# Optimization experiments

Measured on AMD Instinct MI355X. Metric: run time of the kernel, lower is better.

## Reference

```python
import jax, jax.numpy as jnp
import numpy as np

DEPTH = 6; HEADS = 6; DIM = 384; HD = DIM // HEADS
WS = 14; WINDOW_BLOCKS = (0, 1, 3, 4)
IMG = 512; PATCH = 16; GRID = IMG // PATCH        # 32x32 token grid
PRE_GRID = 14                                      # 224 // 16 pretrain grid
SCALE = HD ** -0.5


def layer_norm(x, w, b, eps=1e-5):
    u = x.mean(-1, keepdims=True)
    s = ((x - u) ** 2).mean(-1, keepdims=True)
    return (x - u) / jnp.sqrt(s + eps) * w + b


def get_rel_pos(size, rel_pos):
    # q_size == k_size here; relative coords in [0, 2*size-2]
    coords = jnp.arange(size)[:, None] - jnp.arange(size)[None, :] + (size - 1)
    return rel_pos[coords]  # (size, size, HD)


def attention(x, qkv_w, qkv_b, proj_w, proj_b, rel_h, rel_w):
    B, H, W, C = x.shape
    N = H * W
    qkv = (x.reshape(B, N, C) @ qkv_w.T + qkv_b).reshape(B, N, 3, HEADS, HD)
    qkv = jnp.moveaxis(qkv, 2, 0).transpose(0, 1, 3, 2, 4)  # (3,B,h,N,d)
    q, k, v = qkv[0], qkv[1], qkv[2]
    attn = jnp.einsum('bhqd,bhkd->bhqk', q * SCALE, k)
    # decomposed relative position bias (ViTDet add_decomposed_rel_pos)
    Rh = get_rel_pos(H, rel_h)  # (H,H,d)
    Rw = get_rel_pos(W, rel_w)  # (W,W,d)
    rq = q.reshape(B, HEADS, H, W, HD)
    bias_h = jnp.einsum('bnhwc,hkc->bnhwk', rq, Rh)  # (B,h,H,W,H)
    bias_w = jnp.einsum('bnhwc,wkc->bnhwk', rq, Rw)  # (B,h,H,W,W)
    attn = (attn.reshape(B, HEADS, H, W, H, W)
            + bias_h[..., :, None] + bias_w[..., None, :]).reshape(B, HEADS, N, N)
    attn = jax.nn.softmax(attn, axis=-1)
    out = jnp.einsum('bhqk,bhkd->bhqd', attn, v)
    out = out.transpose(0, 2, 1, 3).reshape(B, H, W, C)
    return out @ proj_w.T + proj_b


def window_partition(x, ws):
    B, H, W, C = x.shape
    pad_h = (ws - H % ws) % ws
    pad_w = (ws - W % ws) % ws
    x = jnp.pad(x, ((0, 0), (0, pad_h), (0, pad_w), (0, 0)))
    Hp, Wp = H + pad_h, W + pad_w
    x = x.reshape(B, Hp // ws, ws, Wp // ws, ws, C)
    x = x.transpose(0, 1, 3, 2, 4, 5).reshape(-1, ws, ws, C)
    return x, Hp, Wp


def window_unpartition(win, ws, Hp, Wp, H, W):
    B = win.shape[0] // ((Hp // ws) * (Wp // ws))
    x = win.reshape(B, Hp // ws, Wp // ws, ws, ws, -1)
    x = x.transpose(0, 1, 3, 2, 4, 5).reshape(B, Hp, Wp, -1)
    return x[:, :H, :W]


def block(x, p, windowed):
    shortcut = x
    x = layer_norm(x, p['n1w'], p['n1b'])
    if windowed:
        H, W = x.shape[1], x.shape[2]
        x, Hp, Wp = window_partition(x, WS)
    x = attention(x, p['qw'], p['qb'], p['pw'], p['pb'], p['rh'], p['rw'])
    if windowed:
        x = window_unpartition(x, WS, Hp, Wp, H, W)
    x = shortcut + x
    h = layer_norm(x, p['n2w'], p['n2b'])
    h = jax.nn.gelu(h @ p['f1w'].T + p['f1b'], approximate=False)
    return x + h @ p['f2w'].T + p['f2b']


def vit_forward(x, patch_w, patch_b, pos_embed, norm1_w, norm1_b, qkv_w, qkv_b,
                proj_w, proj_b, norm2_w, norm2_b, fc1_w, fc1_b, fc2_w, fc2_b,
                rel_pos_h, rel_pos_w):
    y = jax.lax.conv_general_dilated(
        x, patch_w, (PATCH, PATCH), 'VALID',
        dimension_numbers=('NCHW', 'OIHW', 'NCHW'))
    y = y.transpose(0, 2, 3, 1) + patch_b  # (B, GRID, GRID, DIM)
    # abs pos embed: bicubic resize from pretrain 14x14 grid to 32x32
    pos = pos_embed.reshape(1, PRE_GRID, PRE_GRID, DIM)
    pos = jax.image.resize(pos, (1, GRID, GRID, DIM), 'bicubic')
    y = y + pos
    for i in range(DEPTH):
        windowed = i in WINDOW_BLOCKS
        L = 2 * WS - 1 if windowed else 2 * GRID - 1
        p = dict(n1w=norm1_w[i], n1b=norm1_b[i], qw=qkv_w[i], qb=qkv_b[i],
                 pw=proj_w[i], pb=proj_b[i], rh=rel_pos_h[i, :L], rw=rel_pos_w[i, :L],
                 n2w=norm2_w[i], n2b=norm2_b[i], f1w=fc1_w[i], f1b=fc1_b[i],
                 f2w=fc2_w[i], f2b=fc2_b[i])
        y = block(y, p, windowed)
    return y.transpose(0, 3, 1, 2)  # (B, DIM, GRID, GRID) 'last_feat'


def setup_inputs() -> dict:
    key = jax.random.key(0)
    ks = jax.random.split(key, 10)
    B = 4
    std = 0.02
    f32 = jnp.float32
    return {
        'x': jax.random.normal(ks[0], (B, 3, IMG, IMG), f32),
        'patch_w': jax.random.normal(ks[1], (DIM, 3, PATCH, PATCH), f32) * 0.05,
        'patch_b': jnp.zeros((DIM,), f32),
        'pos_embed': jax.random.normal(ks[2], (1, PRE_GRID * PRE_GRID, DIM), f32) * std,
        'norm1_w': jnp.ones((DEPTH, DIM), f32),
        'norm1_b': jnp.zeros((DEPTH, DIM), f32),
        'qkv_w': jax.random.normal(ks[3], (DEPTH, 3 * DIM, DIM), f32) * std,
        'qkv_b': jnp.zeros((DEPTH, 3 * DIM), f32),
        'proj_w': jax.random.normal(ks[4], (DEPTH, DIM, DIM), f32) * std,
        'proj_b': jnp.zeros((DEPTH, DIM), f32),
        'norm2_w': jnp.ones((DEPTH, DIM), f32),
        'norm2_b': jnp.zeros((DEPTH, DIM), f32),
        'fc1_w': jax.random.normal(ks[5], (DEPTH, 4 * DIM, DIM), f32) * std,
        'fc1_b': jnp.zeros((DEPTH, 4 * DIM), f32),
        'fc2_w': jax.random.normal(ks[6], (DEPTH, DIM, 4 * DIM), f32) * std,
        'fc2_b': jnp.zeros((DEPTH, DIM), f32),
        'rel_pos_h': jax.random.normal(ks[7], (DEPTH, 2 * GRID - 1, HD), f32) * std,
        'rel_pos_w': jax.random.normal(ks[8], (DEPTH, 2 * GRID - 1, HD), f32) * std,
    }


def reference(x, patch_w, patch_b, pos_embed, norm1_w, norm1_b, qkv_w, qkv_b,
              proj_w, proj_b, norm2_w, norm2_b, fc1_w, fc1_b, fc2_w, fc2_b,
              rel_pos_h, rel_pos_w):
    return vit_forward(x, patch_w, patch_b, pos_embed, norm1_w, norm1_b, qkv_w, qkv_b,
                       proj_w, proj_b, norm2_w, norm2_b, fc1_w, fc1_b, fc2_w, fc2_b,
                       rel_pos_h, rel_pos_w)
```

## Files before the change

### kernel.cpp

```cpp
#include <hip/hip_runtime.h>
#include <math.h>

#define B_SZ 4
#define DIM 384
#define HEADS 6
#define HD 64
#define NTOK 4096
#define WS 14
#define NWIN 36
#define WTOK 196

typedef unsigned short u16;
typedef __bf16 bf16_t;
typedef bf16_t bf16x8 __attribute__((ext_vector_type(8)));
typedef float f32x4 __attribute__((ext_vector_type(4)));

__device__ __forceinline__ float bf2f(unsigned u) { return __uint_as_float(u << 16); }
__device__ __forceinline__ u16 f2bf(float f) {
    unsigned u = __float_as_uint(f);
    unsigned r = (u + 0x7fffu + ((u >> 16) & 1u)) >> 16;
    return (u16)r;
}

__device__ __forceinline__ void ldsload16(const u16* g, u16* l) {
    __builtin_amdgcn_global_load_lds(
        (const __attribute__((address_space(1))) unsigned int*)g,
        (__attribute__((address_space(3))) unsigned int*)l, 16, 0, 0);
}

__device__ __forceinline__ int swz(int r) { return (r ^ (r >> 2)) & 3; }

__global__ __launch_bounds__(256) void w2b_all_kernel(
        const float* __restrict__ p0, const float* __restrict__ p1,
        const float* __restrict__ p2, const float* __restrict__ p3,
        const float* __restrict__ p4, const float* __restrict__ p5,
        u16* __restrict__ d) {
    int i = blockIdx.x * 256 + threadIdx.x;
    const float* s; int off;
    if      (i <   294912) { s = p0; off = 0; }
    else if (i <  2949120) { s = p1; off = 294912; }
    else if (i <  3833856) { s = p2; off = 2949120; }
    else if (i <  7372800) { s = p3; off = 3833856; }
    else if (i < 10911744) { s = p4; off = 7372800; }
    else if (i < 10918656) { s = p5; off = 10911744; }
    else return;
    d[i] = f2bf(s[i - off]);
}

__global__ __launch_bounds__(256) void im2col_kernel(const float* __restrict__ x,
                                                     u16* __restrict__ col) {
    size_t idx = (size_t)blockIdx.x * 256 + threadIdx.x;
    if (idx >= (size_t)NTOK * 768) return;
    int kk = (int)(idx % 768);
    int p  = (int)(idx / 768);
    int b  = p / 1024;
    int ph = (p % 1024) / 32;
    int pw = p % 32;
    int c = kk / 256;
    int r = kk % 256;
    int i = r / 16, j = r % 16;
    col[idx] = f2bf(x[(size_t)b * 3 * 512 * 512 + (size_t)c * 512 * 512 +
                      (size_t)(ph * 16 + i) * 512 + (pw * 16 + j)]);
}

__device__ inline float cubic_keys(float x) {
    x = fabsf(x);
    if (x <= 1.f) return ((1.5f * x - 2.5f) * x) * x + 1.f;
    if (x < 2.f)  return ((-0.5f * x + 2.5f) * x - 4.f) * x + 2.f;
    return 0.f;
}

__global__ __launch_bounds__(256) void pos_resize_kernel(const float* __restrict__ pe,
                                                         float* __restrict__ posr) {
    int idx = blockIdx.x * 256 + threadIdx.x;
    if (idx >= 1024 * 384) return;
    int c = idx % 384;
    int g = idx / 384;
    int gy = g / 32, gx = g % 32;
    float wy[14], wx[14];
    float sy = (gy + 0.5f) * (14.f / 32.f) - 0.5f;
    float sx = (gx + 0.5f) * (14.f / 32.f) - 0.5f;
    float toty = 0.f, totx = 0.f;
    #pragma unroll
    for (int k = 0; k < 14; ++k) {
        wy[k] = cubic_keys(sy - (float)k); toty += wy[k];
        wx[k] = cubic_keys(sx - (float)k); totx += wx[k];
    }
    float val = 0.f;
    #pragma unroll 1
    for (int iy = 0; iy < 14; ++iy) {
        if (wy[iy] == 0.f) continue;
        float row = 0.f;
        for (int ix = 0; ix < 14; ++ix) {
            if (wx[ix] == 0.f) continue;
            row += wx[ix] * pe[(iy * 14 + ix) * 384 + c];
        }
        val += wy[iy] * row;
    }
    posr[idx] = val / (toty * totx);
}

__global__ __launch_bounds__(64) void epi_ln_kernel(const float* __restrict__ P,
        const float* __restrict__ bias, const float* __restrict__ posr,
        float* __restrict__ y, int addy, int nsk,
        const float* __restrict__ lw, const float* __restrict__ lb,
        u16* __restrict__ lnout, float* __restrict__ outT)
{
    int tok = blockIdx.x, t = threadIdx.x;
    size_t base = (size_t)tok * 384;
    float v[6];
    float s = 0.f;
    #pragma unroll
    for (int i = 0; i < 6; ++i) {
        int c = t + 64 * i;
        float val = bias[c];
        #pragma unroll 1
        for (int sk = 0; sk < nsk; ++sk)
            val += P[(size_t)sk * 1572864 + base + c];
        if (posr) val += posr[(size_t)(tok & 1023) * 384 + c];
        if (addy) val += y[base + c];
        v[i] = val; s += val;
    }
    if (outT) {
        int b = tok >> 10, g = tok & 1023;
        #pragma unroll
        for (int i = 0; i < 6; ++i) {
            int c = t + 64 * i;
            outT[((size_t)(b * 384 + c)) * 1024 + g] = v[i];
        }
        return;
    }
    #pragma unroll
    for (int i = 0; i < 6; ++i) y[base + t + 64 * i] = v[i];
    if (!lnout) return;
    #pragma unroll
    for (int off = 32; off > 0; off >>= 1) s += __shfl_xor(s, off);
    float mean = s * (1.f / 384.f);
    float vs = 0.f;
    #pragma unroll
    for (int i = 0; i < 6; ++i) { float d = v[i] - mean; vs += d * d; }
    #pragma unroll
    for (int off = 32; off > 0; off >>= 1) vs += __shfl_xor(vs, off);
    float inv = rsqrtf(vs * (1.f / 384.f) + 1e-5f);
    u16* orow = lnout + base;
    #pragma unroll
    for (int i = 0; i < 6; ++i) {
        int c = t + 64 * i;
        orow[c] = f2bf((v[i] - mean) * inv * lw[c] + lb[c]);
    }
}

__global__ __launch_bounds__(256) void mfma_gemm3(
        const u16* __restrict__ A, const u16* __restrict__ Wt,
        const float* __restrict__ bias,
        float* __restrict__ outf, u16* __restrict__ outb,
        float* __restrict__ outp,
        int M, int N, int K, int act, int ksplit)
{
    __shared__ u16 As[8192];
    __shared__ u16 Bs[4096];
    int t = threadIdx.x;
    int lane = t & 63, wave = t >> 6;
    int wm = (wave >> 1) * 64, wn = (wave & 1) * 32;
    int m0 = blockIdx.y * 128, n0 = blockIdx.x * 64;
    int ks = blockIdx.z * ksplit, ke = ks + ksplit;

    int r0 = t >> 2,        c0 = ((t & 3) ^ swz(t >> 2)) * 8;
    int r1 = 64 + (t >> 2), c1 = ((t & 3) ^ swz(64 + (t >> 2))) * 8;
    const u16* a0 = A + (size_t)(m0 + r0) * K + c0;
    const u16* a1 = A + (size_t)(m0 + r1) * K + c1;
    const u16* b0 = Wt + (size_t)(n0 + r0) * K + c0;
    u16* asd0 = &As[wave * 512];
    u16* asd1 = &As[2048 + wave * 512];
    u16* bsd0 = &Bs[wave * 512];

    f32x4 acc[4][2] = {};
    int row_a = wm + (lane & 15);
    int row_b = wn + (lane & 15);
    int lq = lane >> 4;

    for (int k0 = ks; k0 < ke; k0 += 64) {
        ldsload16(a0 + k0, asd0);
        ldsload16(a1 + k0, asd1);
        ldsload16(b0 + k0, bsd0);
        ldsload16(a0 + k0 + 32, asd0 + 4096);
        ldsload16(a1 + k0 + 32, asd1 + 4096);
        ldsload16(b0 + k0 + 32, bsd0 + 2048);
        __syncthreads();
        #pragma unroll
        for (int hf = 0; hf < 2; ++hf) {
            bf16x8 af[4], bfr[2];
            #pragma unroll
            for (int i = 0; i < 4; ++i) {
                int r = row_a + i * 16;
                af[i] = *(const bf16x8*)&As[hf * 4096 + r * 32 + ((lq ^ swz(r)) * 8)];
            }
            #pragma unroll
            for (int j = 0; j < 2; ++j) {
                int r = row_b + j * 16;
                bfr[j] = *(const bf16x8*)&Bs[hf * 2048 + r * 32 + ((lq ^ swz(r)) * 8)];
            }
            #pragma unroll
            for (int i = 0; i < 4; ++i)
                #pragma unroll
                for (int j = 0; j < 2; ++j)
                    acc[i][j] = __builtin_amdgcn_mfma_f32_16x16x32_bf16(
                        af[i], bfr[j], acc[i][j], 0, 0, 0);
        }
        __syncthreads();
    }

    int colq = lane & 15, rowq = (lane >> 4) * 4;
    if (outp) {
        float* pp = outp + (size_t)blockIdx.z * M * N;
        #pragma unroll
        for (int i = 0; i < 4; ++i) {
            #pragma unroll
            for (int rr = 0; rr < 4; ++rr) {
                int m = m0 + wm + i * 16 + rowq + rr;
                size_t mo = (size_t)m * N;
                #pragma unroll
                for (int j = 0; j < 2; ++j) {
                    int n = n0 + wn + j * 16 + colq;
                    pp[mo + n] = acc[i][j][rr];
                }
            }
        }
        return;
    }
    #pragma unroll
    for (int i = 0; i < 4; ++i) {
        #pragma unroll
        for (int rr = 0; rr < 4; ++rr) {
            int m = m0 + wm + i * 16 + rowq + rr;
            size_t mo = (size_t)m * N;
            #pragma unroll
            for (int j = 0; j < 2; ++j) {
                int n = n0 + wn + j * 16 + colq;
                float v = acc[i][j][rr] + bias[n];
                if (act)  v = 0.5f * v * (1.f + erff(v * 0.70710678118654752f));
                if (outf) outf[mo + n] = v;
                if (outb) outb[mo + n] = f2bf(v);
            }
        }
    }
}

template<int N, int W>
__global__ __launch_bounds__(256) void attn_mfma(const u16* __restrict__ qkv,
        const u16* __restrict__ qkb, const float* __restrict__ rh,
        const float* __restrict__ rw, u16* __restrict__ outb)
{
    constexpr int JS = (W == 32) ? 64 : 32;
    constexpr int L  = (W == 32) ? 63 : 27;
    constexpr int CTR = W - 1;
    __shared__ u16 KV[7168];
    __shared__ u16 bhl[64 * 66];
    __shared__ u16 bwl[64 * 66];
    __shared__ u16 Qt[64 * 66];

    u16* Ks = KV;
    u16* Vt = KV + 2048;
    u16* Pb = KV + 4608;
    u16* Rt = KV;

    int t = threadIdx.x, lane = t & 63, wave = t >> 6;
    int quad = lane >> 4, l15 = lane & 15;
    int uh = blockIdx.x, qb0 = blockIdx.y * 64;
    int h = uh % HEADS, u = uh / HEADS;
    size_t tbase = (size_t)u * 1024;
    int wb_ = u / 9, wr = u - wb_ * 9;
    int wy = wr / 3, wx = wr - wy * 3;

    auto rowptr = [&](int lq) -> const u16* {
        if constexpr (W == 32) {
            return qkv + (tbase + lq) * 1152;
        } else {
            int iy = lq / WS, ix = lq - iy * WS;
            int gy = wy * WS + iy, gx = wx * WS + ix;
            if (gy < 32 || gx < 32) {
                if (gy < 32 && gx < 32)
                    return qkv + (size_t)(wb_ * 1024 + gy * 32 + gx) * 1152;
            }
            return qkb;
        }
    };

    {
        int q = t & 63, ch0 = (t >> 6) * 16;
        int qc = qb0 + q; if (qc >= N) qc = N - 1;
        const u16* qp = rowptr(qc) + h * 64 + ch0;
        uint4 a = *(const uint4*)qp;
        uint4 b = *(const uint4*)(qp + 8);
        u16 vals[16];
        *(uint4*)vals = a; *(uint4*)(vals + 8) = b;
        #pragma unroll
        for (int c = 0; c < 16; ++c)
            Qt[(ch0 + c) * 66 + q] = ((qb0 + q) < N) ? vals[c] : (u16)0;
    }

    #pragma unroll
    for (int table = 0; table < 2; ++table) {
        __syncthreads();
        const float* tab = table ? rw : rh;
        for (int idx = t; idx < JS * 8; idx += 256) {
            int j = idx >> 3, cc0 = (idx & 7) * 8;
            u16 tmp[8];
            if (j < L) {
                const float* src = tab + (size_t)j * 64 + cc0;
                #pragma unroll
                for (int c = 0; c < 8; ++c) tmp[c] = f2bf(src[c]);
            } else {
                #pragma unroll
                for (int c = 0; c < 8; ++c) tmp[c] = 0;
            }
            *(uint4*)&Rt[j * 72 + cc0] = *(uint4*)tmp;
        }
        __syncthreads();
        if (wave < JS / 16) {
            int jt = wave;
            bf16x8 af0 = *(const bf16x8*)&Rt[(jt * 16 + l15) * 72 + quad * 8];
            bf16x8 af1 = *(const bf16x8*)&Rt[(jt * 16 + l15) * 72 + 32 + quad * 8];
            u16* dst = table ? bwl : bhl;
            #pragma unroll
            for (int qt = 0; qt < 4; ++qt) {
                bf16x8 qf0, qf1;
                u16* p0 = (u16*)&qf0; u16* p1 = (u16*)&qf1;
                #pragma unroll
                for (int z = 0; z < 8; ++z) {
                    p0[z] = Qt[(quad * 8 + z) * 66 + qt * 16 + l15];
                    p1[z] = Qt[(32 + quad * 8 + z) * 66 + qt * 16 + l15];
                }
                f32x4 acc = {};
                acc = __builtin_amdgcn_mfma_f32_16x16x32_bf16(af0, qf0, acc, 0, 0, 0);
                acc = __builtin_amdgcn_mfma_f32_16x16x32_bf16(af1, qf1, acc, 0, 0, 0);
                #pragma unroll
                for (int r = 0; r < 4; ++r)
                    dst[(qt * 16 + l15) * 66 + jt * 16 + quad * 4 + r] = f2bf(acc[r]);
            }
        }
    }
    __syncthreads();

    bf16x8 qf[2];
    #pragma unroll
    for (int hc = 0; hc < 2; ++hc) {
        u16* qv = (u16*)&qf[hc];
        #pragma unroll
        for (int j = 0; j < 8; ++j)
            qv[j] = Qt[(hc * 32 + quad * 8 + j) * 66 + wave * 16 + l15];
    }
    int qme = wave * 16 + l15;
    int qq = qb0 + qme; if (qq >= N) qq = N - 1;
    int qh = qq / W, qw = qq - qh * W;
    float bwreg[2][4];
    if constexpr (W == 32) {
        #pragma unroll
        for (int kc2 = 0; kc2 < 2; ++kc2)
            #pragma unroll
            for (int r = 0; r < 4; ++r) {
                int keyl = kc2 * 16 + quad * 4 + r;
                bwreg[kc2][r] = bf2f(bwl[qme * 66 + (qw - keyl + CTR)]);
            }
    }

    f32x4 of[4] = {};
    float lsum = 0.f;
    constexpr int NKT = (N + 31) / 32;

    for (int kt = 0; kt < NKT; ++kt) {
        int kb = kt * 32;
        __syncthreads();
        {
            int p = wave * 64 + lane;
            int key = p >> 3;
            int c8 = (p & 7) ^ (key & 7);
            int kc = kb + key; if (kc >= N) kc = N - 1;
            ldsload16(rowptr(kc) + 384 + h * 64 + c8 * 8, &Ks[wave * 512]);
        }
        {
            int k = t & 31, ch0 = (t >> 5) * 8;
            int kc = kb + k; if (kc >= N) kc = N - 1;
            const u16* vp = rowptr(kc) + 768 + h * 64 + ch0;
            uint4 vv = *(const uint4*)vp;
            u16 tmp[8]; *(uint4*)tmp = vv;
            #pragma unroll
            for (int c = 0; c < 8; ++c) Vt[(ch0 + c) * 40 + k] = tmp[c];
        }
        __syncthreads();

        f32x4 st[2] = {};
        #pragma unroll
        for (int hc = 0; hc < 2; ++hc) {
            #pragma unroll
            for (int kc2 = 0; kc2 < 2; ++kc2) {
                int key = kc2 * 16 + l15;
                int c8 = hc * 4 + quad;
                int p = key * 8 + (c8 ^ (key & 7));
                bf16x8 kf = *(const bf16x8*)&Ks[p * 8];
                st[kc2] = __builtin_amdgcn_mfma_f32_16x16x32_bf16(
                    kf, qf[hc], st[kc2], 0, 0, 0);
            }
        }
        float bh_t = 0.f;
        if constexpr (W == 32) bh_t = bf2f(bhl[qme * 66 + (qh - (kb >> 5) + CTR)]);
        #pragma unroll
        for (int kc2 = 0; kc2 < 2; ++kc2) {
            #pragma unroll
            for (int r = 0; r < 4; ++r) {
                int keyl = kc2 * 16 + quad * 4 + r;
                int key = kb + keyl;
                float b;
                if constexpr (W == 32) {
                    b = bh_t + bwreg[kc2][r];
                } else {
                    int kk2 = (key < N) ? key : (N - 1);
                    int kh = kk2 / W, kw = kk2 - kh * W;
                    b = bf2f(bhl[qme * 66 + (qh - kh + CTR)]) +
                        bf2f(bwl[qme * 66 + (qw - kw + CTR)]);
                }
                float p = __expf(fmaf(st[kc2][r], 0.125f, b));
                if (key >= N) p = 0.f;
                lsum += p;
                Pb[wave * 640 + l15 * 40 + keyl] = f2bf(p);
            }
        }
        bf16x8 pf = *(const bf16x8*)&Pb[wave * 640 + l15 * 40 + quad * 8];
        #pragma unroll
        for (int ca = 0; ca < 4; ++ca) {
            bf16x8 vf = *(const bf16x8*)&Vt[(ca * 16 + l15) * 40 + quad * 8];
            of[ca] = __builtin_amdgcn_mfma_f32_16x16x32_bf16(
                vf, pf, of[ca], 0, 0, 0);
        }
    }

    lsum += __shfl_xor(lsum, 16);
    lsum += __shfl_xor(lsum, 32);
    float inv = 1.f / lsum;
    int q = qb0 + qme;
    if (q < N) {
        u16* op;
        if constexpr (W == 32) {
            op = outb + (tbase + q) * 384 + h * 64;
        } else {
            int iy = q / WS, ix = q - iy * WS;
            int gy = wy * WS + iy, gx = wx * WS + ix;
            if (gy >= 32 || gx >= 32) return;
            op = outb + (size_t)(wb_ * 1024 + gy * 32 + gx) * 384 + h * 64;
        }
        #pragma unroll
        for (int ca = 0; ca < 4; ++ca)
            #pragma unroll
            for (int r = 0; r < 4; ++r)
                op[ca * 16 + quad * 4 + r] = f2bf(of[ca][r] * inv);
    }
}

static inline void launch_gemm(const u16* A, const u16* W, const float* bias,
                               float* outf, u16* outb,
                               int M, int N, int K, int act, hipStream_t s) {
    dim3 g(N / 64, M / 128, 1);
    mfma_gemm3<<<g, 256, 0, s>>>(A, W, bias, outf, outb, nullptr, M, N, K, act, K);
}

static inline void launch_gemm_sk(const u16* A, const u16* W, float* P,
                                  int M, int N, int K, int SK, hipStream_t s) {
    dim3 g(N / 64, M / 128, SK);
    mfma_gemm3<<<g, 256, 0, s>>>(A, W, nullptr, nullptr, nullptr, P,
                                 M, N, K, 0, K / SK);
}

extern "C" void kernel_launch(void* const* d_in, const int* in_sizes, int n_in,
                              void* d_out, int out_size, void* d_ws, size_t ws_size,
                              hipStream_t stream) {
    const float* x      = (const float*)d_in[0];
    const float* patchw = (const float*)d_in[1];
    const float* patchb = (const float*)d_in[2];
    const float* pos    = (const float*)d_in[3];
    const float* n1w    = (const float*)d_in[4];
    const float* n1b    = (const float*)d_in[5];
    const float* qkvw   = (const float*)d_in[6];
    const float* qkvb   = (const float*)d_in[7];
    const float* pw     = (const float*)d_in[8];
    const float* pb     = (const float*)d_in[9];
    const float* n2w    = (const float*)d_in[10];
    const float* n2b    = (const float*)d_in[11];
    const float* f1w    = (const float*)d_in[12];
    const float* f1b    = (const float*)d_in[13];
    const float* f2w    = (const float*)d_in[14];
    const float* f2b    = (const float*)d_in[15];
    const float* rph    = (const float*)d_in[16];
    const float* rpw    = (const float*)d_in[17];
    float* out = (float*)d_out;

    float* y   = (float*)d_ws;
    u16* attb  = (u16*)(y + 1572864);
    u16* mlpb  = attb + 1572864;
    u16* lnb   = mlpb + 6291456;
    u16* qkvx  = lnb + 1572864;
    u16* rsrv  = qkvx + 4718592;
    u16* wb    = rsrv + 7864320;
    float* posr = (float*)(wb + 10918656);

    u16* colb  = rsrv;
    float* P_patch = (float*)attb;
    float* P_pf    = (float*)qkvx;

    u16* wb_patch = wb;
    u16* wb_qkv   = wb + 294912;
    u16* wb_pw    = wb + 2949120;
    u16* wb_f1    = wb + 3833856;
    u16* wb_f2    = wb + 7372800;
    u16* wqb      = wb + 10911744;

    w2b_all_kernel<<<(10918656 + 255) / 256, 256, 0, stream>>>(
        patchw, qkvw, pw, f1w, f2w, qkvb, wb);
    pos_resize_kernel<<<1536, 256, 0, stream>>>(pos, posr);

    {
        size_t tot = (size_t)NTOK * 768;
        im2col_kernel<<<(int)((tot + 255) / 256), 256, 0, stream>>>(x, colb);
        launch_gemm_sk(colb, wb_patch, P_patch, NTOK, 384, 768, 2, stream);
        epi_ln_kernel<<<NTOK, 64, 0, stream>>>(P_patch, patchb, posr, y, 0, 2,
                                               n1w, n1b, lnb, nullptr);
    }

    for (int i = 0; i < 6; ++i) {
        bool windowed = (i == 0 || i == 1 || i == 3 || i == 4);
        const float* rh = rph + (size_t)i * 63 * 64;
        const float* rw = rpw + (size_t)i * 63 * 64;
        launch_gemm(lnb, wb_qkv + (size_t)i * 442368, qkvb + i * 1152,
                    nullptr, qkvx, NTOK, 1152, 384, 0, stream);
        if (windowed) {
            attn_mfma<WTOK, WS><<<dim3(NWIN * HEADS, 4), 256, 0, stream>>>(
                qkvx, wqb + i * 1152, rh, rw, attb);
        } else {
            attn_mfma<1024, 32><<<dim3(B_SZ * HEADS, 16), 256, 0, stream>>>(
                qkvx, wqb + i * 1152, rh, rw, attb);
        }
        launch_gemm_sk(attb, wb_pw + (size_t)i * 147456, P_pf,
                       NTOK, 384, 384, 2, stream);
        epi_ln_kernel<<<NTOK, 64, 0, stream>>>(P_pf, pb + i * 384, nullptr, y, 1, 2,
                                               n2w + i * 384, n2b + i * 384, lnb,
                                               nullptr);
        launch_gemm(lnb, wb_f1 + (size_t)i * 589824, f1b + i * 1536,
                    nullptr, mlpb, NTOK, 1536, 384, 1, stream);
        launch_gemm_sk(mlpb, wb_f2 + (size_t)i * 589824, P_pf,
                       NTOK, 384, 1536, 4, stream);
        if (i < 5)
            epi_ln_kernel<<<NTOK, 64, 0, stream>>>(P_pf, f2b + i * 384, nullptr, y,
                                                   1, 4, n1w + (i + 1) * 384,
                                                   n1b + (i + 1) * 384, lnb, nullptr);
        else
            epi_ln_kernel<<<NTOK, 64, 0, stream>>>(P_pf, f2b + i * 384, nullptr, y,
                                                   1, 4, nullptr, nullptr, nullptr,
                                                   out);
    }
}
```

Before: 797.8 us.

## Double-buffer K/V tiles in attention, merge setup kernels, reduce fc2 split-K

The attention kernel now double-buffers its K and V tiles in shared memory. The next tile's K is issued via global_load_lds and V is prefetched into registers while the current tile is computed, leaving one barrier per iteration instead of two. The weight-conversion, positional-resize and im2col kernels are merged into a single launch to cut launch overhead. The fc2 split-K factor drops from 4 to 2, which halves partial-sum traffic but gives the GEMM fewer blocks, and the larger LDS footprint may lower attention occupancy.

After: 775.6 us. 2.8% less time.

```diff
diff --git a/kernel.cpp b/kernel.cpp
--- a/kernel.cpp
+++ b/kernel.cpp
@@ -30,39 +30,6 @@
 
 __device__ __forceinline__ int swz(int r) { return (r ^ (r >> 2)) & 3; }
 
-__global__ __launch_bounds__(256) void w2b_all_kernel(
-        const float* __restrict__ p0, const float* __restrict__ p1,
-        const float* __restrict__ p2, const float* __restrict__ p3,
-        const float* __restrict__ p4, const float* __restrict__ p5,
-        u16* __restrict__ d) {
-    int i = blockIdx.x * 256 + threadIdx.x;
-    const float* s; int off;
-    if      (i <   294912) { s = p0; off = 0; }
-    else if (i <  2949120) { s = p1; off = 294912; }
-    else if (i <  3833856) { s = p2; off = 2949120; }
-    else if (i <  7372800) { s = p3; off = 3833856; }
-    else if (i < 10911744) { s = p4; off = 7372800; }
-    else if (i < 10918656) { s = p5; off = 10911744; }
-    else return;
-    d[i] = f2bf(s[i - off]);
-}
-
-__global__ __launch_bounds__(256) void im2col_kernel(const float* __restrict__ x,
-                                                     u16* __restrict__ col) {
-    size_t idx = (size_t)blockIdx.x * 256 + threadIdx.x;
-    if (idx >= (size_t)NTOK * 768) return;
-    int kk = (int)(idx % 768);
-    int p  = (int)(idx / 768);
-    int b  = p / 1024;
-    int ph = (p % 1024) / 32;
-    int pw = p % 32;
-    int c = kk / 256;
-    int r = kk % 256;
-    int i = r / 16, j = r % 16;
-    col[idx] = f2bf(x[(size_t)b * 3 * 512 * 512 + (size_t)c * 512 * 512 +
-                      (size_t)(ph * 16 + i) * 512 + (pw * 16 + j)]);
-}
-
 __device__ inline float cubic_keys(float x) {
     x = fabsf(x);
     if (x <= 1.f) return ((1.5f * x - 2.5f) * x) * x + 1.f;
@@ -70,34 +37,66 @@
     return 0.f;
 }
 
-__global__ __launch_bounds__(256) void pos_resize_kernel(const float* __restrict__ pe,
-                                                         float* __restrict__ posr) {
-    int idx = blockIdx.x * 256 + threadIdx.x;
-    if (idx >= 1024 * 384) return;
-    int c = idx % 384;
-    int g = idx / 384;
-    int gy = g / 32, gx = g % 32;
-    float wy[14], wx[14];
-    float sy = (gy + 0.5f) * (14.f / 32.f) - 0.5f;
-    float sx = (gx + 0.5f) * (14.f / 32.f) - 0.5f;
-    float toty = 0.f, totx = 0.f;
-    #pragma unroll
-    for (int k = 0; k < 14; ++k) {
-        wy[k] = cubic_keys(sy - (float)k); toty += wy[k];
-        wx[k] = cubic_keys(sx - (float)k); totx += wx[k];
-    }
-    float val = 0.f;
-    #pragma unroll 1
-    for (int iy = 0; iy < 14; ++iy) {
-        if (wy[iy] == 0.f) continue;
-        float row = 0.f;
-        for (int ix = 0; ix < 14; ++ix) {
-            if (wx[ix] == 0.f) continue;
-            row += wx[ix] * pe[(iy * 14 + ix) * 384 + c];
-        }
-        val += wy[iy] * row;
-    }
-    posr[idx] = val / (toty * totx);
+__global__ __launch_bounds__(256) void setup_kernel(
+        const float* __restrict__ p0, const float* __restrict__ p1,
+        const float* __restrict__ p2, const float* __restrict__ p3,
+        const float* __restrict__ p4, const float* __restrict__ p5,
+        u16* __restrict__ wb, const float* __restrict__ pe,
+        float* __restrict__ posr, const float* __restrict__ x,
+        u16* __restrict__ col) {
+    int i = blockIdx.x * 256 + threadIdx.x;
+    if (i < 10918656) {
+        const float* s; int off;
+        if      (i <   294912) { s = p0; off = 0; }
+        else if (i <  2949120) { s = p1; off = 294912; }
+        else if (i <  3833856) { s = p2; off = 2949120; }
+        else if (i <  7372800) { s = p3; off = 3833856; }
+        else if (i < 10911744) { s = p4; off = 7372800; }
+        else                   { s = p5; off = 10911744; }
+        wb[i] = f2bf(s[i - off]);
+        return;
+    }
+    i -= 10918656;
+    if (i < 393216) {
+        int c = i % 384;
+        int g = i / 384;
+        int gy = g / 32, gx = g % 32;
+        float wy[14], wx[14];
+        float sy = (gy + 0.5f) * (14.f / 32.f) - 0.5f;
+        float sx = (gx + 0.5f) * (14.f / 32.f) - 0.5f;
+        float toty = 0.f, totx = 0.f;
+        #pragma unroll
+        for (int k = 0; k < 14; ++k) {
+            wy[k] = cubic_keys(sy - (float)k); toty += wy[k];
+            wx[k] = cubic_keys(sx - (float)k); totx += wx[k];
+        }
+        float val = 0.f;
+        #pragma unroll 1
+        for (int iy = 0; iy < 14; ++iy) {
+            if (wy[iy] == 0.f) continue;
+            float row = 0.f;
+            for (int ix = 0; ix < 14; ++ix) {
+                if (wx[ix] == 0.f) continue;
+                row += wx[ix] * pe[(iy * 14 + ix) * 384 + c];
+            }
+            val += wy[iy] * row;
+        }
+        posr[i] = val / (toty * totx);
+        return;
+    }
+    i -= 393216;
+    {
+        int kk = i % 768;
+        int p  = i / 768;
+        int b  = p / 1024;
+        int ph = (p % 1024) / 32;
+        int pw = p % 32;
+        int c = kk / 256;
+        int r = kk % 256;
+        int ii = r / 16, j = r % 16;
+        col[i] = f2bf(x[(size_t)b * 3 * 512 * 512 + (size_t)c * 512 * 512 +
+                        (size_t)(ph * 16 + ii) * 512 + (pw * 16 + j)]);
+    }
 }
 
 __global__ __launch_bounds__(64) void epi_ln_kernel(const float* __restrict__ P,
@@ -254,14 +253,12 @@
     constexpr int JS = (W == 32) ? 64 : 32;
     constexpr int L  = (W == 32) ? 63 : 27;
     constexpr int CTR = W - 1;
-    __shared__ u16 KV[7168];
+    __shared__ u16 KV[11776];
     __shared__ u16 bhl[64 * 66];
     __shared__ u16 bwl[64 * 66];
     __shared__ u16 Qt[64 * 66];
 
-    u16* Ks = KV;
-    u16* Vt = KV + 2048;
-    u16* Pb = KV + 4608;
+    u16* Pb = KV + 9216;
     u16* Rt = KV;
 
     int t = threadIdx.x, lane = t & 63, wave = t >> 6;
@@ -272,16 +269,14 @@
     int wb_ = u / 9, wr = u - wb_ * 9;
     int wy = wr / 3, wx = wr - wy * 3;
 
-    auto rowptr = [&](int lq) -> const u16* {
+    auto rowptr = [&](int lq2) -> const u16* {
         if constexpr (W == 32) {
-            return qkv + (tbase + lq) * 1152;
+            return qkv + (tbase + lq2) * 1152;
         } else {
-            int iy = lq / WS, ix = lq - iy * WS;
+            int iy = lq2 / WS, ix = lq2 - iy * WS;
             int gy = wy * WS + iy, gx = wx * WS + ix;
-            if (gy < 32 || gx < 32) {
-                if (gy < 32 && gx < 32)
-                    return qkv + (size_t)(wb_ * 1024 + gy * 32 + gx) * 1152;
-            }
+            if (gy < 32 && gx < 32)
+                return qkv + (size_t)(wb_ * 1024 + gy * 32 + gx) * 1152;
             return qkb;
         }
     };
@@ -342,6 +337,21 @@
     }
     __syncthreads();
 
+    constexpr int NKT = (N + 31) / 32;
+    {
+        int pch = wave * 64 + lane;
+        int key = pch >> 3;
+        int c8 = (pch & 7) ^ (key & 7);
+        int kc = key; if (kc >= N) kc = N - 1;
+        ldsload16(rowptr(kc) + 384 + h * 64 + c8 * 8, KV + wave * 512);
+        int k = t & 31, ch0v = (t >> 5) * 8;
+        uint4 vv = *(const uint4*)(rowptr(k) + 768 + h * 64 + ch0v);
+        u16 tmp[8]; *(uint4*)tmp = vv;
+        u16* vdst = KV + 4096;
+        #pragma unroll
+        for (int c = 0; c < 8; ++c) vdst[(ch0v + c) * 40 + k] = tmp[c];
+    }
+
     bf16x8 qf[2];
     #pragma unroll
     for (int hc = 0; hc < 2; ++hc) {
@@ -366,28 +376,27 @@
 
     f32x4 of[4] = {};
     float lsum = 0.f;
-    constexpr int NKT = (N + 31) / 32;
+    __syncthreads();
 
     for (int kt = 0; kt < NKT; ++kt) {
         int kb = kt * 32;
-        __syncthreads();
-        {
-            int p = wave * 64 + lane;
-            int key = p >> 3;
-            int c8 = (p & 7) ^ (key & 7);
-            int kc = kb + key; if (kc >= N) kc = N - 1;
-            ldsload16(rowptr(kc) + 384 + h * 64 + c8 * 8, &Ks[wave * 512]);
-        }
-        {
-            int k = t & 31, ch0 = (t >> 5) * 8;
-            int kc = kb + k; if (kc >= N) kc = N - 1;
-            const u16* vp = rowptr(kc) + 768 + h * 64 + ch0;
-            uint4 vv = *(const uint4*)vp;
-            u16 tmp[8]; *(uint4*)tmp = vv;
-            #pragma unroll
-            for (int c = 0; c < 8; ++c) Vt[(ch0 + c) * 40 + k] = tmp[c];
-        }
-        __syncthreads();
+        int p = kt & 1;
+        const u16* ksp = KV + p * 2048;
+        const u16* vtp = KV + 4096 + p * 2560;
+        bool pref = (kt + 1 < NKT);
+        uint4 vpref;
+        int kpf = t & 31, ch0v = (t >> 5) * 8;
+        if (pref) {
+            int kb2 = kb + 32;
+            int pch = wave * 64 + lane;
+            int key = pch >> 3;
+            int c8 = (pch & 7) ^ (key & 7);
+            int kc = kb2 + key; if (kc >= N) kc = N - 1;
+            ldsload16(rowptr(kc) + 384 + h * 64 + c8 * 8,
+                      KV + (1 - p) * 2048 + wave * 512);
+            int kcv = kb2 + kpf; if (kcv >= N) kcv = N - 1;
+            vpref = *(const uint4*)(rowptr(kcv) + 768 + h * 64 + ch0v);
+        }
 
         f32x4 st[2] = {};
         #pragma unroll
@@ -396,8 +405,8 @@
             for (int kc2 = 0; kc2 < 2; ++kc2) {
                 int key = kc2 * 16 + l15;
                 int c8 = hc * 4 + quad;
-                int p = key * 8 + (c8 ^ (key & 7));
-                bf16x8 kf = *(const bf16x8*)&Ks[p * 8];
+                int pp = key * 8 + (c8 ^ (key & 7));
+                bf16x8 kf = *(const bf16x8*)&ksp[pp * 8];
                 st[kc2] = __builtin_amdgcn_mfma_f32_16x16x32_bf16(
                     kf, qf[hc], st[kc2], 0, 0, 0);
             }
@@ -419,18 +428,26 @@
                     b = bf2f(bhl[qme * 66 + (qh - kh + CTR)]) +
                         bf2f(bwl[qme * 66 + (qw - kw + CTR)]);
                 }
-                float p = __expf(fmaf(st[kc2][r], 0.125f, b));
-                if (key >= N) p = 0.f;
-                lsum += p;
-                Pb[wave * 640 + l15 * 40 + keyl] = f2bf(p);
+                float pv = __expf(fmaf(st[kc2][r], 0.125f, b));
+                if (key >= N) pv = 0.f;
+                lsum += pv;
+                Pb[wave * 640 + l15 * 40 + keyl] = f2bf(pv);
             }
         }
         bf16x8 pf = *(const bf16x8*)&Pb[wave * 640 + l15 * 40 + quad * 8];
         #pragma unroll
         for (int ca = 0; ca < 4; ++ca) {
-            bf16x8 vf = *(const bf16x8*)&Vt[(ca * 16 + l15) * 40 + quad * 8];
+            bf16x8 vf = *(const bf16x8*)&vtp[(ca * 16 + l15) * 40 + quad * 8];
             of[ca] = __builtin_amdgcn_mfma_f32_16x16x32_bf16(
                 vf, pf, of[ca], 0, 0, 0);
+        }
+
+        if (pref) {
+            u16 tmp[8]; *(uint4*)tmp = vpref;
+            u16* vdst = KV + 4096 + (1 - p) * 2560;
+            #pragma unroll
+            for (int c = 0; c < 8; ++c) vdst[(ch0v + c) * 40 + kpf] = tmp[c];
+            __syncthreads();
         }
     }
 
@@ -513,17 +530,12 @@
     u16* wb_f2    = wb + 7372800;
     u16* wqb      = wb + 10911744;
 
-    w2b_all_kernel<<<(10918656 + 255) / 256, 256, 0, stream>>>(
-        patchw, qkvw, pw, f1w, f2w, qkvb, wb);
-    pos_resize_kernel<<<1536, 256, 0, stream>>>(pos, posr);
-
-    {
-        size_t tot = (size_t)NTOK * 768;
-        im2col_kernel<<<(int)((tot + 255) / 256), 256, 0, stream>>>(x, colb);
-        launch_gemm_sk(colb, wb_patch, P_patch, NTOK, 384, 768, 2, stream);
-        epi_ln_kernel<<<NTOK, 64, 0, stream>>>(P_patch, patchb, posr, y, 0, 2,
-                                               n1w, n1b, lnb, nullptr);
-    }
+    setup_kernel<<<(14457600 + 255) / 256, 256, 0, stream>>>(
+        patchw, qkvw, pw, f1w, f2w, qkvb, wb, pos, posr, x, colb);
+
+    launch_gemm_sk(colb, wb_patch, P_patch, NTOK, 384, 768, 2, stream);
+    epi_ln_kernel<<<NTOK, 64, 0, stream>>>(P_patch, patchb, posr, y, 0, 2,
+                                           n1w, n1b, lnb, nullptr);
 
     for (int i = 0; i < 6; ++i) {
         bool windowed = (i == 0 || i == 1 || i == 3 || i == 4);
@@ -546,14 +558,14 @@
         launch_gemm(lnb, wb_f1 + (size_t)i * 589824, f1b + i * 1536,
                     nullptr, mlpb, NTOK, 1536, 384, 1, stream);
         launch_gemm_sk(mlpb, wb_f2 + (size_t)i * 589824, P_pf,
-                       NTOK, 384, 1536, 4, stream);
+                       NTOK, 384, 1536, 2, stream);
         if (i < 5)
             epi_ln_kernel<<<NTOK, 64, 0, stream>>>(P_pf, f2b + i * 384, nullptr, y,
-                                                   1, 4, n1w + (i + 1) * 384,
+                                                   1, 2, n1w + (i + 1) * 384,
                                                    n1b + (i + 1) * 384, lnb, nullptr);
         else
             epi_ln_kernel<<<NTOK, 64, 0, stream>>>(P_pf, f2b + i * 384, nullptr, y,
-                                                   1, 4, nullptr, nullptr, nullptr,
+                                                   1, 2, nullptr, nullptr, nullptr,
                                                    out);
     }
 }
```
